# Optimization experiments

Hardware: AMD Instinct MI355X
Metric: run time of the kernel (lower is better)

Reference implementation:

```python
import jax, jax.numpy as jnp
import numpy as np

X_DIM = 512
Z_DIM = 16
HEADS = 8
DIM_HEAD = 64
INNER = HEADS * DIM_HEAD
EPS = 1e-5


def _layernorm(t, g, b):
    mu = jnp.mean(t, axis=-1, keepdims=True)
    var = jnp.mean(jnp.square(t - mu), axis=-1, keepdims=True)
    return (t - mu) * jax.lax.rsqrt(var + EPS) * g + b


def setup_inputs() -> dict:
    key = jax.random.key(0)
    ks = jax.random.split(key, 8)
    B, N = 4, 2048
    s_x = 1.0 / np.sqrt(X_DIM)
    s_z = 1.0 / np.sqrt(Z_DIM)
    s_i = 1.0 / np.sqrt(INNER)
    return {
        "x": jax.random.normal(ks[0], (B, N, X_DIM), dtype=jnp.float32),
        "z": jax.random.normal(ks[1], (B, 1, Z_DIM), dtype=jnp.float32),
        "ln_x_g": jnp.ones((X_DIM,), jnp.float32),
        "ln_x_b": jnp.zeros((X_DIM,), jnp.float32),
        "ln_z_g": jnp.ones((Z_DIM,), jnp.float32),
        "ln_z_b": jnp.zeros((Z_DIM,), jnp.float32),
        "Wq": jax.random.normal(ks[2], (X_DIM, INNER), jnp.float32) * s_x,
        "Wk": jax.random.normal(ks[3], (X_DIM, INNER), jnp.float32) * s_x,
        "Wv": jax.random.normal(ks[4], (X_DIM, INNER), jnp.float32) * s_x,
        "Wz": jax.random.normal(ks[5], (Z_DIM, 2 * X_DIM), jnp.float32) * s_z,
        "Wo": jax.random.normal(ks[6], (INNER, X_DIM), jnp.float32) * s_i,
        "bo": jnp.zeros((X_DIM,), jnp.float32),
    }


def reference(x, z, ln_x_g, ln_x_b, ln_z_g, ln_z_b, Wq, Wk, Wv, Wz, Wo, bo):
    scale = DIM_HEAD ** (-0.5)
    # z path: LN -> Linear -> SiLU -> split into FiLM scale/shift
    zp = jax.nn.silu(_layernorm(z, ln_z_g, ln_z_b) @ Wz)  # [B, 1, 2*x_dim]
    z1, z2 = jnp.split(zp, 2, axis=-1)
    x_mod = _layernorm(x, ln_x_g, ln_x_b) * z1 + z2       # [B, N, x_dim]
    B, N, _ = x.shape

    def heads(t):  # [B, N, inner] -> [B, h, N, d]
        return t.reshape(B, N, HEADS, DIM_HEAD).transpose(0, 2, 1, 3)

    q = heads(x_mod @ Wq)
    k = heads(x_mod @ Wk)
    v = heads(x_mod @ Wv)
    sim = jnp.einsum('bhid,bhjd->bhij', q, k) * scale
    attn = jax.nn.softmax(sim, axis=-1)
    out = jnp.einsum('bhij,bhjd->bhid', attn, v)           # [B, h, N, d]
    out = out.transpose(0, 2, 1, 3).reshape(B, N, INNER)
    return out @ Wo + bo
```

## Files before the change

kernel.cpp:

```cpp
#include <hip/hip_runtime.h>

#define XD 512
#define HEADS 8
#define DH 64
#define NSEQ 2048
#define NBATCH 4
#define NROWS (NBATCH*NSEQ)

#define SCALE_L2E 0.18033688011112042f
#define DEFER_THR 4.0f

typedef __attribute__((ext_vector_type(8))) short bf16x8;
typedef __attribute__((ext_vector_type(8))) unsigned short u16x8;
typedef __attribute__((ext_vector_type(4))) float f32x4;
typedef __attribute__((ext_vector_type(16))) float f32x16;

__device__ __forceinline__ unsigned short f2bf(float f) {
  union { float f; unsigned u; } v; v.f = f;
  return (unsigned short)((v.u + 0x7fffu + ((v.u >> 16) & 1u)) >> 16);
}

__device__ __forceinline__ float fexp2(float x) {
#if __has_builtin(__builtin_amdgcn_exp2f)
  return __builtin_amdgcn_exp2f(x);
#else
  return exp2f(x);
#endif
}

__device__ __forceinline__ unsigned cvt_pk_bf16(float lo, float hi) {
  unsigned r;
  asm("v_cvt_pk_bf16_f32 %0, %1, %2" : "=v"(r) : "v"(lo), "v"(hi));
  return r;
}

__device__ __forceinline__ void gload_lds16(const unsigned short* g, unsigned short* l) {
  __builtin_amdgcn_global_load_lds(
      (const __attribute__((address_space(1))) unsigned int*)g,
      (__attribute__((address_space(3))) unsigned int*)l, 16, 0, 0);
}

__global__ __launch_bounds__(256) void wtrans4z_kernel(
    const float* __restrict__ W0, const float* __restrict__ W1,
    const float* __restrict__ W2, const float* __restrict__ W3,
    unsigned short* __restrict__ dst,
    const float* __restrict__ z, const float* __restrict__ zg, const float* __restrict__ zb,
    const float* __restrict__ Wz, float* __restrict__ z12) {
  __shared__ float tile[32][33];
  int blk = blockIdx.x;
  if (blk < 1024) {
    int w = blk >> 8;
    int t = blk & 255;
    int tn = t >> 4, tk = t & 15;
    const float* W = (w == 0) ? W0 : (w == 1) ? W1 : (w == 2) ? W2 : W3;
    int r = threadIdx.x >> 5, c = threadIdx.x & 31;
#pragma unroll
    for (int i = 0; i < 4; ++i)
      tile[r + 8 * i][c] = W[(size_t)(tk * 32 + r + 8 * i) * 512 + tn * 32 + c];
    __syncthreads();
    unsigned short* d = dst + (size_t)w * 262144;
#pragma unroll
    for (int i = 0; i < 4; ++i)
      d[(size_t)(tn * 32 + r + 8 * i) * 512 + tk * 32 + c] = f2bf(tile[c][r + 8 * i]);
  } else {
    int bb = blk - 1024;
    int t = threadIdx.x;
    float zv[16];
    float mean = 0.f;
#pragma unroll
    for (int i = 0; i < 16; ++i) { zv[i] = z[bb * 16 + i]; mean += zv[i]; }
    mean *= (1.f / 16.f);
    float var = 0.f;
#pragma unroll
    for (int i = 0; i < 16; ++i) { float d = zv[i] - mean; var += d * d; }
    var *= (1.f / 16.f);
    float rs = rsqrtf(var + 1e-5f);
    float zn[16];
#pragma unroll
    for (int i = 0; i < 16; ++i) zn[i] = (zv[i] - mean) * rs * zg[i] + zb[i];
    for (int c = t; c < 1024; c += 256) {
      float acc = 0.f;
#pragma unroll
      for (int i = 0; i < 16; ++i) acc += zn[i] * Wz[i * 1024 + c];
      float s = acc / (1.f + __expf(-acc));
      z12[bb * 1024 + c] = s;
    }
  }
}

__global__ __launch_bounds__(256) void xmod_kernel(
    const float* __restrict__ x, const float* __restrict__ g, const float* __restrict__ b,
    const float* __restrict__ z12, unsigned short* __restrict__ xm) {
  int wave = threadIdx.x >> 6, lane = threadIdx.x & 63;
  int row = blockIdx.x * 4 + wave;
  const float* xr = x + (size_t)row * XD;
  float4 v0 = ((const float4*)xr)[lane * 2];
  float4 v1 = ((const float4*)xr)[lane * 2 + 1];
  float vv[8] = {v0.x, v0.y, v0.z, v0.w, v1.x, v1.y, v1.z, v1.w};
  float sum = 0.f, sq = 0.f;
#pragma unroll
  for (int i = 0; i < 8; ++i) { sum += vv[i]; sq += vv[i] * vv[i]; }
#pragma unroll
  for (int o = 32; o; o >>= 1) { sum += __shfl_xor(sum, o); sq += __shfl_xor(sq, o); }
  float mean = sum * (1.f / 512.f);
  float var = sq * (1.f / 512.f) - mean * mean;
  float rs = rsqrtf(var + 1e-5f);
  int bb = row >> 11;
  const float* zz = z12 + bb * 1024;
  int c0 = lane * 8;
  u16x8 o8;
#pragma unroll
  for (int i = 0; i < 8; ++i) {
    int c = c0 + i;
    float t = (vv[i] - mean) * rs * g[c] + b[c];
    t = t * zz[c] + zz[512 + c];
    o8[i] = f2bf(t);
  }
  *(u16x8*)(xm + (size_t)row * XD + c0) = o8;
}

__global__ __launch_bounds__(256, 2) void gemm_qkv_kernel(
    const unsigned short* __restrict__ A, const unsigned short* __restrict__ Wt,
    unsigned short* __restrict__ Qo, unsigned short* __restrict__ Ko,
    unsigned short* __restrict__ Vo) {
  __shared__ unsigned short Alds[128 * 64];
  __shared__ unsigned short Blds[128 * 64];
  int widx = threadIdx.x >> 6, lane = threadIdx.x & 63;
  int blk = blockIdx.x;
  int xcd = blk & 7, local = blk >> 3;
  int mt = xcd * 8 + local / 12;
  int nt = local % 12;
  int blkM = mt * 128, blkN = nt * 128;
  int wr = widx >> 1, wc = widx & 1;
  int lr = lane & 15, lg = lane >> 4;
  int srow = lane >> 3, sc8 = lane & 7;

  f32x4 acc[4][4] = {};

  for (int kc = 0; kc < 512; kc += 64) {
#pragma unroll
    for (int i = 0; i < 4; ++i) {
      int rb = widx * 32 + i * 8;
      int row = rb + srow;
      int cs = (sc8 ^ (row & 7)) * 8;
      gload_lds16(A + (size_t)(blkM + row) * 512 + kc + cs, &Alds[rb * 64]);
      gload_lds16(Wt + (size_t)(blkN + row) * 512 + kc + cs, &Blds[rb * 64]);
    }
    __syncthreads();

#pragma unroll
    for (int kh = 0; kh < 2; ++kh) {
      bf16x8 bfr[4];
#pragma unroll
      for (int ni = 0; ni < 4; ++ni) {
        int brow = wc * 64 + ni * 16 + lr;
        bfr[ni] = *(const bf16x8*)&Blds[brow * 64 + (((kh * 4 + lg) ^ (brow & 7)) * 8)];
      }
#pragma unroll
      for (int mi = 0; mi < 4; ++mi) {
        int arow = wr * 64 + mi * 16 + lr;
        bf16x8 afr = *(const bf16x8*)&Alds[arow * 64 + (((kh * 4 + lg) ^ (arow & 7)) * 8)];
#pragma unroll
        for (int ni = 0; ni < 4; ++ni)
          acc[mi][ni] = __builtin_amdgcn_mfma_f32_16x16x32_bf16(afr, bfr[ni], acc[mi][ni], 0, 0, 0);
      }
    }
    __syncthreads();
  }

  int cg = blkN >> 9;
#pragma unroll
  for (int mi = 0; mi < 4; ++mi)
#pragma unroll
    for (int ni = 0; ni < 4; ++ni) {
      int col = blkN + wc * 64 + ni * 16 + lr;
      int c = col & 511;
#pragma unroll
      for (int j = 0; j < 4; ++j) {
        int row = blkM + wr * 64 + mi * 16 + lg * 4 + j;
        float v = acc[mi][ni][j];
        if (cg == 0) {
          Qo[(size_t)row * 512 + c] = f2bf(v * SCALE_L2E);
        } else if (cg == 1) {
          Ko[(size_t)row * 512 + c] = f2bf(v);
        } else {
          int bb = row >> 11, n = row & 2047, h = c >> 6, d = c & 63;
          int j4 = n & 15;
          int slot = (j4 & 3) | (((j4 >> 3) & 1) << 2) | (((j4 >> 2) & 1) << 3);
          int np = (n & ~15) | slot;
          Vo[(((size_t)(bb * HEADS + h) * DH + d) << 11) + np] = f2bf(v);
        }
      }
    }
}

__global__ __launch_bounds__(256, 2) void gemm_out_kernel(
    const unsigned short* __restrict__ A, const unsigned short* __restrict__ Wt,
    float* __restrict__ out, const float* __restrict__ bias) {
  __shared__ unsigned short Alds[128 * 64];
  __shared__ unsigned short Blds[64 * 64];
  int widx = threadIdx.x >> 6, lane = threadIdx.x & 63;
  int blk = blockIdx.x;
  int xcd = blk & 7, local = blk >> 3;
  int mt = xcd * 8 + (local >> 3);
  int nt = local & 7;
  int blkM = mt * 128, blkN = nt * 64;
  int wr = widx >> 1, wc = widx & 1;
  int lr = lane & 15, lg = lane >> 4;
  int srow = lane >> 3, sc8 = lane & 7;

  f32x4 acc[4][2] = {};

  for (int kc = 0; kc < 512; kc += 64) {
#pragma unroll
    for (int i = 0; i < 4; ++i) {
      int rb = widx * 32 + i * 8;
      int row = rb + srow;
      int cs = (sc8 ^ (row & 7)) * 8;
      gload_lds16(A + (size_t)(blkM + row) * 512 + kc + cs, &Alds[rb * 64]);
    }
#pragma unroll
    for (int i = 0; i < 2; ++i) {
      int rb = widx * 16 + i * 8;
      int row = rb + srow;
      int cs = (sc8 ^ (row & 7)) * 8;
      gload_lds16(Wt + (size_t)(blkN + row) * 512 + kc + cs, &Blds[rb * 64]);
    }
    __syncthreads();

#pragma unroll
    for (int kh = 0; kh < 2; ++kh) {
      bf16x8 bfr[2];
#pragma unroll
      for (int ni = 0; ni < 2; ++ni) {
        int brow = wc * 32 + ni * 16 + lr;
        bfr[ni] = *(const bf16x8*)&Blds[brow * 64 + (((kh * 4 + lg) ^ (brow & 7)) * 8)];
      }
#pragma unroll
      for (int mi = 0; mi < 4; ++mi) {
        int arow = wr * 64 + mi * 16 + lr;
        bf16x8 afr = *(const bf16x8*)&Alds[arow * 64 + (((kh * 4 + lg) ^ (arow & 7)) * 8)];
#pragma unroll
        for (int ni = 0; ni < 2; ++ni)
          acc[mi][ni] = __builtin_amdgcn_mfma_f32_16x16x32_bf16(afr, bfr[ni], acc[mi][ni], 0, 0, 0);
      }
    }
    __syncthreads();
  }

#pragma unroll
  for (int mi = 0; mi < 4; ++mi)
#pragma unroll
    for (int ni = 0; ni < 2; ++ni) {
      int col = blkN + wc * 32 + ni * 16 + lr;
#pragma unroll
      for (int j = 0; j < 4; ++j) {
        int row = blkM + wr * 64 + mi * 16 + lg * 4 + j;
        out[(size_t)row * 512 + col] = acc[mi][ni][j] + bias[col];
      }
    }
}


#define AKV 64
#define NCH_S 16

#define STAGE_S(buf, kcc) do {                                            \
    unsigned short* dK = skm + (buf) * 8192 + wq * (16 * 64);             \
    gload_lds16(gkA + (size_t)(kcc) * 512, dK);                           \
    gload_lds16(gkB + (size_t)(kcc) * 512, dK + 8 * 64);                  \
    gload_lds16(gvA + (kcc), dK + 4096);                                  \
    gload_lds16(gvB + (kcc), dK + 4096 + 8 * 64);                         \
  } while (0)

#define PROC(b) do {                                                      \
    f32x16 s[2];                                                          \
    __builtin_amdgcn_s_setprio(1);                                        \
    _Pragma("unroll")                                                     \
    for (int kt = 0; kt < 2; ++kt) {                                      \
      f32x16 z = {};                                                      \
      _Pragma("unroll")                                                   \
      for (int ks = 0; ks < 4; ++ks) {                                    \
        bf16x8 kf = *(const bf16x8*)(sk + ko[kt * 4 + ks] + (b) * 8192);  \
        z = __builtin_amdgcn_mfma_f32_32x32x16_bf16(kf, qf[ks], z, 0, 0, 0); \
      }                                                                   \
      s[kt] = z;                                                          \
    }                                                                     \
    __builtin_amdgcn_s_setprio(0);                                        \
                                \
    float q4[8];                                                          \
    _Pragma("unroll")                                                     \
    for (int i = 0; i < 8; ++i)                                           \
      q4[i] = fmaxf(fmaxf(s[0][i], s[0][i + 8]), fmaxf(s[1][i], s[1][i + 8])); \
    float m8 = fmaxf(fmaxf(fmaxf(q4[0], q4[1]), fmaxf(q4[2], q4[3])),     \
                     fmaxf(fmaxf(q4[4], q4[5]), fmaxf(q4[6], q4[7])));    \
    m8 = fmaxf(m8, __shfl_xor(m8, 32));                                   \
    bool grow = (m8 > m0 + DEFER_THR);                                    \
    if (__any((int)grow)) {                                               \
      float mn = fmaxf(m0, m8);                                           \
      float al = fexp2(m0 - mn);                                          \
      m0 = mn; l0 *= al;                                                  \
      _Pragma("unroll")                                                   \
      for (int dt = 0; dt < 2; ++dt)                                      \
        _Pragma("unroll")                                                 \
        for (int j = 0; j < 16; ++j) o[dt][j] *= al;                      \
    }                                                                     \
    float p0[16], p1[16]; float rsA = 0.f, rsB = 0.f;                     \
    _Pragma("unroll")                                                     \
    for (int i = 0; i < 16; ++i) { p0[i] = fexp2(s[0][i] - m0); rsA += p0[i]; } \
    _Pragma("unroll")                                                     \
    for (int i = 0; i < 16; ++i) { p1[i] = fexp2(s[1][i] - m0); rsB += p1[i]; } \
    float rs = rsA + rsB;                                                 \
    rs += __shfl_xor(rs, 32);                                             \
    l0 += rs;                                                             \
    union { unsigned w[4]; bf16x8 v; } pf[4];                             \
    _Pragma("unroll")                                                     \
    for (int d2 = 0; d2 < 4; ++d2) {                                      \
      pf[0].w[d2] = cvt_pk_bf16(p0[2 * d2], p0[2 * d2 + 1]);              \
      pf[1].w[d2] = cvt_pk_bf16(p0[8 + 2 * d2], p0[8 + 2 * d2 + 1]);      \
      pf[2].w[d2] = cvt_pk_bf16(p1[2 * d2], p1[2 * d2 + 1]);              \
      pf[3].w[d2] = cvt_pk_bf16(p1[8 + 2 * d2], p1[8 + 2 * d2 + 1]);      \
    }                                                                     \
    __builtin_amdgcn_s_setprio(1);                                        \
    _Pragma("unroll")                                                     \
    for (int dt = 0; dt < 2; ++dt) {                                      \
      f32x16 acc = o[dt];                                                 \
      _Pragma("unroll")                                                   \
      for (int g = 0; g < 4; ++g) {                                       \
        bf16x8 vf = *(const bf16x8*)(sk + vo[dt * 4 + g] + (b) * 8192);   \
        acc = __builtin_amdgcn_mfma_f32_32x32x16_bf16(vf, pf[g].v, acc, 0, 0, 0); \
      }                                                                   \
      o[dt] = acc;                                                        \
    }                                                                     \
    __builtin_amdgcn_s_setprio(0);                                        \
  } while (0)

__global__ __launch_bounds__(512, 4) void attn_kernel(
    const unsigned short* __restrict__ Q, const unsigned short* __restrict__ K,
    const unsigned short* __restrict__ VT, unsigned short* __restrict__ O) {
  __shared__ __align__(16) unsigned short SH[2][4][4096];
  int tid = threadIdx.x;
  int widx = tid >> 6, lane = tid & 63;
  int strm = widx >> 2;
  int wq = widx & 3;
  int blk = blockIdx.x;
  int xcd = blk & 7;
  int idx = blk >> 3;
  int bh = xcd * 4 + (idx >> 4);
  int qg = idx & 15;
  int b = bh >> 3, h = bh & 7;
  int ql = lane & 31, hi = lane >> 5;
  int qrow0 = qg * 128 + wq * 32;

  bf16x8 qf[4];
  const unsigned short* Qp = Q + (size_t)(b * NSEQ + qrow0 + ql) * 512 + h * 64 + hi * 8;
#pragma unroll
  for (int ks = 0; ks < 4; ++ks) qf[ks] = *(const bf16x8*)(Qp + ks * 16);

  const unsigned short* Kg = K + (size_t)b * NSEQ * 512 + h * 64 + (size_t)strm * 1024 * 512;
  const unsigned short* Vg = VT + (size_t)bh * DH * NSEQ + strm * 1024;

  const unsigned short* sk = &SH[strm][0][0];
  unsigned short* skm = &SH[strm][0][0];
  int srA = wq * 16 + (lane >> 3), srB = srA + 8;
  int csA = (lane & 7) ^ (srA & 7), csB = (lane & 7) ^ (srB & 7);
  const unsigned short* gkA = Kg + (size_t)srA * 512 + csA * 8;
  const unsigned short* gkB = Kg + (size_t)srB * 512 + csB * 8;
  const unsigned short* gvA = Vg + (size_t)srA * NSEQ + csA * 8;
  const unsigned short* gvB = Vg + (size_t)srB * NSEQ + csB * 8;
  unsigned ko[8], vo[8];
#pragma unroll
  for (int kt = 0; kt < 2; ++kt)
#pragma unroll
    for (int ks = 0; ks < 4; ++ks) {
      int krow = kt * 32 + ql;
      ko[kt * 4 + ks] = krow * 64 + (((ks * 2 + hi) ^ (krow & 7)) * 8);
    }
#pragma unroll
  for (int dt = 0; dt < 2; ++dt)
#pragma unroll
    for (int g = 0; g < 4; ++g) {
      int vrow = dt * 32 + ql;
      vo[dt * 4 + g] = 4096 + vrow * 64 + (((g * 2 + hi) ^ (vrow & 7)) * 8);
    }

  float m0 = -3.0e38f, l0 = 0.f;
  f32x16 o[2] = {};

  STAGE_S(0, 0);
  __syncthreads();
  for (int tt = 0; tt < NCH_S; tt += 2) {
    if (tt + 1 < NCH_S) STAGE_S(1, (tt + 1) * AKV);
    PROC(0);
    __syncthreads();
    if (tt + 2 < NCH_S) STAGE_S(0, (tt + 2) * AKV);
    PROC(1);
    __syncthreads();
  }

  float* sm = (float*)&SH[0][0][0];
  if (strm == 1) {
    int base = (wq * 64 + lane) * 34;
    sm[base] = m0;
    sm[base + 1] = l0;
#pragma unroll
    for (int j = 0; j < 16; ++j) { sm[base + 2 + j] = o[0][j]; sm[base + 18 + j] = o[1][j]; }
  }
  __syncthreads();
  if (strm == 0) {
    int base = (wq * 64 + lane) * 34;
    float mB = sm[base], lB = sm[base + 1];
    float mN = fmaxf(m0, mB);
    float aA = fexp2(m0 - mN), aB = fexp2(mB - mN);
    float inv = 1.f / (l0 * aA + lB * aB);
    float aAi = aA * inv, aBi = aB * inv;
    size_t rowb = (size_t)(b * NSEQ + qrow0 + ql) * 512 + h * 64 + hi * 4;
#pragma unroll
    for (int dt = 0; dt < 2; ++dt)
#pragma unroll
      for (int c = 0; c < 8; ++c) {
        float vlo = o[dt][2 * c] * aAi + sm[base + 2 + dt * 16 + 2 * c] * aBi;
        float vhi = o[dt][2 * c + 1] * aAi + sm[base + 2 + dt * 16 + 2 * c + 1] * aBi;
        unsigned w = cvt_pk_bf16(vlo, vhi);
        int d0 = dt * 32 + 8 * (c >> 1) + (c & 1) * 2;
        *(unsigned*)(O + rowb + d0) = w;
      }
  }
}

extern "C" void kernel_launch(void* const* d_in, const int* in_sizes, int n_in,
                              void* d_out, int out_size, void* d_ws, size_t ws_size,
                              hipStream_t stream) {
  const float* x   = (const float*)d_in[0];
  const float* z   = (const float*)d_in[1];
  const float* lxg = (const float*)d_in[2];
  const float* lxb = (const float*)d_in[3];
  const float* lzg = (const float*)d_in[4];
  const float* lzb = (const float*)d_in[5];
  const float* Wq  = (const float*)d_in[6];
  const float* Wk  = (const float*)d_in[7];
  const float* Wv  = (const float*)d_in[8];
  const float* Wz  = (const float*)d_in[9];
  const float* Wo  = (const float*)d_in[10];
  const float* bo  = (const float*)d_in[11];

  char* ws = (char*)d_ws;
  unsigned short* xm  = (unsigned short*)(ws);
  unsigned short* qb  = (unsigned short*)(ws + 8388608);
  unsigned short* kb  = (unsigned short*)(ws + 16777216);
  unsigned short* vt  = (unsigned short*)(ws + 25165824);
  unsigned short* ao  = (unsigned short*)(ws + 33554432);
  unsigned short* wqt = (unsigned short*)(ws + 41943040);
  unsigned short* wot = (unsigned short*)(ws + 43515904);
  float*          z12 = (float*)(ws + 44040192);

  wtrans4z_kernel<<<1028, 256, 0, stream>>>(Wq, Wk, Wv, Wo, wqt, z, lzg, lzb, Wz, z12);
  xmod_kernel<<<NROWS / 4, 256, 0, stream>>>(x, lxg, lxb, z12, xm);
  gemm_qkv_kernel<<<768, 256, 0, stream>>>(xm, wqt, qb, kb, vt);
  attn_kernel<<<512, 512, 0, stream>>>(qb, kb, vt, ao);
  gemm_out_kernel<<<512, 256, 0, stream>>>(ao, wot, (float*)d_out, bo);
}
```

Before: 95.15 us.

## Process two query tiles per wave in attention to reuse K/V LDS fragments

```diff
diff --git a/kernel.cpp b/kernel.cpp
--- a/kernel.cpp
+++ b/kernel.cpp
@@ -274,68 +274,81 @@
   } while (0)
 
 #define PROC(b) do {                                                      \
-    f32x16 s[2];                                                          \
+    f32x16 s[2][2];                                                       \
     __builtin_amdgcn_s_setprio(1);                                        \
     _Pragma("unroll")                                                     \
     for (int kt = 0; kt < 2; ++kt) {                                      \
-      f32x16 z = {};                                                      \
-      _Pragma("unroll")                                                   \
-      for (int ks = 0; ks < 4; ++ks) {                                    \
-        bf16x8 kf = *(const bf16x8*)(sk + ko[kt * 4 + ks] + (b) * 8192);  \
-        z = __builtin_amdgcn_mfma_f32_32x32x16_bf16(kf, qf[ks], z, 0, 0, 0); \
+      bf16x8 kf[4];                                                       \
+      _Pragma("unroll")                                                   \
+      for (int ks = 0; ks < 4; ++ks)                                      \
+        kf[ks] = *(const bf16x8*)(sk + ko[kt * 4 + ks] + (b) * 8192);     \
+      _Pragma("unroll")                                                   \
+      for (int qt = 0; qt < 2; ++qt) {                                    \
+        f32x16 z = {};                                                    \
+        _Pragma("unroll")                                                 \
+        for (int ks = 0; ks < 4; ++ks)                                    \
+          z = __builtin_amdgcn_mfma_f32_32x32x16_bf16(kf[ks], qf[qt][ks], z, 0, 0, 0); \
+        s[qt][kt] = z;                                                    \
       }                                                                   \
-      s[kt] = z;                                                          \
     }                                                                     \
     __builtin_amdgcn_s_setprio(0);                                        \
-                                \
-    float q4[8];                                                          \
+    union { unsigned w[4]; bf16x8 v; } pf[2][4];                          \
     _Pragma("unroll")                                                     \
-    for (int i = 0; i < 8; ++i)                                           \
-      q4[i] = fmaxf(fmaxf(s[0][i], s[0][i + 8]), fmaxf(s[1][i], s[1][i + 8])); \
-    float m8 = fmaxf(fmaxf(fmaxf(q4[0], q4[1]), fmaxf(q4[2], q4[3])),     \
-                     fmaxf(fmaxf(q4[4], q4[5]), fmaxf(q4[6], q4[7])));    \
-    m8 = fmaxf(m8, __shfl_xor(m8, 32));                                   \
-    bool grow = (m8 > m0 + DEFER_THR);                                    \
-    if (__any((int)grow)) {                                               \
-      float mn = fmaxf(m0, m8);                                           \
-      float al = fexp2(m0 - mn);                                          \
-      m0 = mn; l0 *= al;                                                  \
-      _Pragma("unroll")                                                   \
-      for (int dt = 0; dt < 2; ++dt)                                      \
+    for (int qt = 0; qt < 2; ++qt) {                                      \
+      float q4[8];                                                        \
+      _Pragma("unroll")                                                   \
+      for (int i = 0; i < 8; ++i)                                         \
+        q4[i] = fmaxf(fmaxf(s[qt][0][i], s[qt][0][i + 8]),                \
+                      fmaxf(s[qt][1][i], s[qt][1][i + 8]));               \
+      float m8 = fmaxf(fmaxf(fmaxf(q4[0], q4[1]), fmaxf(q4[2], q4[3])),   \
+                       fmaxf(fmaxf(q4[4], q4[5]), fmaxf(q4[6], q4[7])));  \
+      m8 = fmaxf(m8, __shfl_xor(m8, 32));                                 \
+      bool grow = (m8 > m0[qt] + DEFER_THR);                              \
+      if (__any((int)grow)) {                                             \
+        float mn = fmaxf(m0[qt], m8);                                     \
+        float al = fexp2(m0[qt] - mn);                                    \
+        m0[qt] = mn; l0[qt] *= al;                                        \
         _Pragma("unroll")                                                 \
-        for (int j = 0; j < 16; ++j) o[dt][j] *= al;                      \
-    }                                                                     \
-    float p0[16], p1[16]; float rsA = 0.f, rsB = 0.f;                     \
-    _Pragma("unroll")                                                     \
-    for (int i = 0; i < 16; ++i) { p0[i] = fexp2(s[0][i] - m0); rsA += p0[i]; } \
-    _Pragma("unroll")                                                     \
-    for (int i = 0; i < 16; ++i) { p1[i] = fexp2(s[1][i] - m0); rsB += p1[i]; } \
-    float rs = rsA + rsB;                                                 \
-    rs += __shfl_xor(rs, 32);                                             \
-    l0 += rs;                                                             \
-    union { unsigned w[4]; bf16x8 v; } pf[4];                             \
-    _Pragma("unroll")                                                     \
-    for (int d2 = 0; d2 < 4; ++d2) {                                      \
-      pf[0].w[d2] = cvt_pk_bf16(p0[2 * d2], p0[2 * d2 + 1]);              \
-      pf[1].w[d2] = cvt_pk_bf16(p0[8 + 2 * d2], p0[8 + 2 * d2 + 1]);      \
-      pf[2].w[d2] = cvt_pk_bf16(p1[2 * d2], p1[2 * d2 + 1]);              \
-      pf[3].w[d2] = cvt_pk_bf16(p1[8 + 2 * d2], p1[8 + 2 * d2 + 1]);      \
+        for (int dt = 0; dt < 2; ++dt)                                    \
+          _Pragma("unroll")                                               \
+          for (int j = 0; j < 16; ++j) o[qt][dt][j] *= al;                \
+      }                                                                   \
+      float p0[16], p1[16]; float rsA = 0.f, rsB = 0.f;                   \
+      _Pragma("unroll")                                                   \
+      for (int i = 0; i < 16; ++i) { p0[i] = fexp2(s[qt][0][i] - m0[qt]); rsA += p0[i]; } \
+      _Pragma("unroll")                                                   \
+      for (int i = 0; i < 16; ++i) { p1[i] = fexp2(s[qt][1][i] - m0[qt]); rsB += p1[i]; } \
+      float rs = rsA + rsB;                                               \
+      rs += __shfl_xor(rs, 32);                                           \
+      l0[qt] += rs;                                                       \
+      _Pragma("unroll")                                                   \
+      for (int d2 = 0; d2 < 4; ++d2) {                                    \
+        pf[qt][0].w[d2] = cvt_pk_bf16(p0[2 * d2], p0[2 * d2 + 1]);        \
+        pf[qt][1].w[d2] = cvt_pk_bf16(p0[8 + 2 * d2], p0[8 + 2 * d2 + 1]);\
+        pf[qt][2].w[d2] = cvt_pk_bf16(p1[2 * d2], p1[2 * d2 + 1]);        \
+        pf[qt][3].w[d2] = cvt_pk_bf16(p1[8 + 2 * d2], p1[8 + 2 * d2 + 1]);\
+      }                                                                   \
     }                                                                     \
     __builtin_amdgcn_s_setprio(1);                                        \
     _Pragma("unroll")                                                     \
     for (int dt = 0; dt < 2; ++dt) {                                      \
-      f32x16 acc = o[dt];                                                 \
-      _Pragma("unroll")                                                   \
-      for (int g = 0; g < 4; ++g) {                                       \
-        bf16x8 vf = *(const bf16x8*)(sk + vo[dt * 4 + g] + (b) * 8192);   \
-        acc = __builtin_amdgcn_mfma_f32_32x32x16_bf16(vf, pf[g].v, acc, 0, 0, 0); \
+      bf16x8 vf[4];                                                       \
+      _Pragma("unroll")                                                   \
+      for (int g = 0; g < 4; ++g)                                         \
+        vf[g] = *(const bf16x8*)(sk + vo[dt * 4 + g] + (b) * 8192);       \
+      _Pragma("unroll")                                                   \
+      for (int qt = 0; qt < 2; ++qt) {                                    \
+        f32x16 acc = o[qt][dt];                                           \
+        _Pragma("unroll")                                                 \
+        for (int g = 0; g < 4; ++g)                                       \
+          acc = __builtin_amdgcn_mfma_f32_32x32x16_bf16(vf[g], pf[qt][g].v, acc, 0, 0, 0); \
+        o[qt][dt] = acc;                                                  \
       }                                                                   \
-      o[dt] = acc;                                                        \
     }                                                                     \
     __builtin_amdgcn_s_setprio(0);                                        \
   } while (0)
 
-__global__ __launch_bounds__(512, 4) void attn_kernel(
+__global__ __launch_bounds__(512, 2) void attn_kernel(
     const unsigned short* __restrict__ Q, const unsigned short* __restrict__ K,
     const unsigned short* __restrict__ VT, unsigned short* __restrict__ O) {
   __shared__ __align__(16) unsigned short SH[2][4][4096];
@@ -346,16 +359,19 @@
   int blk = blockIdx.x;
   int xcd = blk & 7;
   int idx = blk >> 3;
-  int bh = xcd * 4 + (idx >> 4);
-  int qg = idx & 15;
+  int bh = xcd * 4 + (idx >> 3);
+  int qg = idx & 7;
   int b = bh >> 3, h = bh & 7;
   int ql = lane & 31, hi = lane >> 5;
-  int qrow0 = qg * 128 + wq * 32;
-
-  bf16x8 qf[4];
+  int qrow0 = qg * 256 + wq * 64;
+
+  bf16x8 qf[2][4];
   const unsigned short* Qp = Q + (size_t)(b * NSEQ + qrow0 + ql) * 512 + h * 64 + hi * 8;
 #pragma unroll
-  for (int ks = 0; ks < 4; ++ks) qf[ks] = *(const bf16x8*)(Qp + ks * 16);
+  for (int qt = 0; qt < 2; ++qt)
+#pragma unroll
+    for (int ks = 0; ks < 4; ++ks)
+      qf[qt][ks] = *(const bf16x8*)(Qp + (size_t)qt * 32 * 512 + ks * 16);
 
   const unsigned short* Kg = K + (size_t)b * NSEQ * 512 + h * 64 + (size_t)strm * 1024 * 512;
   const unsigned short* Vg = VT + (size_t)bh * DH * NSEQ + strm * 1024;
@@ -384,8 +400,9 @@
       vo[dt * 4 + g] = 4096 + vrow * 64 + (((g * 2 + hi) ^ (vrow & 7)) * 8);
     }
 
-  float m0 = -3.0e38f, l0 = 0.f;
-  f32x16 o[2] = {};
+  float m0[2] = {-3.0e38f, -3.0e38f};
+  float l0[2] = {0.f, 0.f};
+  f32x16 o[2][2] = {};
 
   STAGE_S(0, 0);
   __syncthreads();
@@ -399,32 +416,39 @@
   }
 
   float* sm = (float*)&SH[0][0][0];
-  if (strm == 1) {
-    int base = (wq * 64 + lane) * 34;
-    sm[base] = m0;
-    sm[base + 1] = l0;
-#pragma unroll
-    for (int j = 0; j < 16; ++j) { sm[base + 2 + j] = o[0][j]; sm[base + 18 + j] = o[1][j]; }
-  }
-  __syncthreads();
-  if (strm == 0) {
-    int base = (wq * 64 + lane) * 34;
-    float mB = sm[base], lB = sm[base + 1];
-    float mN = fmaxf(m0, mB);
-    float aA = fexp2(m0 - mN), aB = fexp2(mB - mN);
-    float inv = 1.f / (l0 * aA + lB * aB);
-    float aAi = aA * inv, aBi = aB * inv;
-    size_t rowb = (size_t)(b * NSEQ + qrow0 + ql) * 512 + h * 64 + hi * 4;
-#pragma unroll
-    for (int dt = 0; dt < 2; ++dt)
-#pragma unroll
-      for (int c = 0; c < 8; ++c) {
-        float vlo = o[dt][2 * c] * aAi + sm[base + 2 + dt * 16 + 2 * c] * aBi;
-        float vhi = o[dt][2 * c + 1] * aAi + sm[base + 2 + dt * 16 + 2 * c + 1] * aBi;
-        unsigned w = cvt_pk_bf16(vlo, vhi);
-        int d0 = dt * 32 + 8 * (c >> 1) + (c & 1) * 2;
-        *(unsigned*)(O + rowb + d0) = w;
-      }
+#pragma unroll 1
+  for (int qt = 0; qt < 2; ++qt) {
+    if (strm == 1) {
+      int base = (wq * 64 + lane) * 34;
+      sm[base] = m0[qt];
+      sm[base + 1] = l0[qt];
+#pragma unroll
+      for (int j = 0; j < 16; ++j) {
+        sm[base + 2 + j] = o[qt][0][j];
+        sm[base + 18 + j] = o[qt][1][j];
+      }
+    }
+    __syncthreads();
+    if (strm == 0) {
+      int base = (wq * 64 + lane) * 34;
+      float mB = sm[base], lB = sm[base + 1];
+      float mN = fmaxf(m0[qt], mB);
+      float aA = fexp2(m0[qt] - mN), aB = fexp2(mB - mN);
+      float inv = 1.f / (l0[qt] * aA + lB * aB);
+      float aAi = aA * inv, aBi = aB * inv;
+      size_t rowb = (size_t)(b * NSEQ + qrow0 + qt * 32 + ql) * 512 + h * 64 + hi * 4;
+#pragma unroll
+      for (int dt = 0; dt < 2; ++dt)
+#pragma unroll
+        for (int c = 0; c < 8; ++c) {
+          float vlo = o[qt][dt][2 * c] * aAi + sm[base + 2 + dt * 16 + 2 * c] * aBi;
+          float vhi = o[qt][dt][2 * c + 1] * aAi + sm[base + 2 + dt * 16 + 2 * c + 1] * aBi;
+          unsigned w = cvt_pk_bf16(vlo, vhi);
+          int d0 = dt * 32 + 8 * (c >> 1) + (c & 1) * 2;
+          *(unsigned*)(O + rowb + d0) = w;
+        }
+    }
+    __syncthreads();
   }
 }
 
@@ -457,6 +481,6 @@
   wtrans4z_kernel<<<1028, 256, 0, stream>>>(Wq, Wk, Wv, Wo, wqt, z, lzg, lzb, Wz, z12);
   xmod_kernel<<<NROWS / 4, 256, 0, stream>>>(x, lxg, lxb, z12, xm);
   gemm_qkv_kernel<<<768, 256, 0, stream>>>(xm, wqt, qb, kb, vt);
-  attn_kernel<<<512, 512, 0, stream>>>(qb, kb, vt, ao);
+  attn_kernel<<<256, 512, 0, stream>>>(qb, kb, vt, ao);
   gemm_out_kernel<<<512, 256, 0, stream>>>(ao, wot, (float*)d_out, bo);
 }
```

After: 207.5 us. 118% more time.
